# Performance work log

Hardware: AMD Instinct MI355X
Metric: run time of the kernel (lower is better)

Reference implementation:

```python
import jax, jax.numpy as jnp
import numpy as np

N = 100000   # nodes
E = 1600000  # edges
D = 128      # in_dim
H = 128      # hidden_dim
C = 40       # num_classes
EPS = 1e-5   # LayerNorm eps (torch default)


def setup_inputs() -> dict:
    key = jax.random.key(0)
    ks = jax.random.split(key, 16)
    x = jax.random.normal(ks[0], (N, D), dtype=jnp.float32)
    edge_index = jax.random.randint(ks[1], (2, E), 0, N, dtype=jnp.int64)
    s = 1.0 / np.sqrt(D)
    inp = {"x": x, "edge_index": edge_index}
    # 3 GCN layers: weight [in, H], bias [H]; LayerNorm gamma/beta [H]
    for i in range(3):
        inp[f"W{i}"] = jax.random.normal(ks[2 + i], (D if i == 0 else H, H), dtype=jnp.float32) * s
        inp[f"b{i}"] = jnp.zeros((H,), jnp.float32)
        inp[f"g{i}"] = jnp.ones((H,), jnp.float32)
        inp[f"be{i}"] = jnp.zeros((H,), jnp.float32)
    inp["Wc"] = jax.random.normal(ks[10], (H, C), dtype=jnp.float32) * (1.0 / np.sqrt(H))
    inp["bc"] = jnp.zeros((C,), jnp.float32)
    return inp


def _layer_norm(h, g, b):
    mu = jnp.mean(h, axis=-1, keepdims=True)
    var = jnp.var(h, axis=-1, keepdims=True)  # biased, matches torch
    return (h - mu) * jax.lax.rsqrt(var + EPS) * g + b


def _gcn_conv(x, W, b, src, dst, enorm, dinv2):
    # GCNConv: D^{-1/2}(A+I)D^{-1/2} X W + b (self-loops handled analytically)
    h = x @ W                                   # [N, H]
    agg = jax.ops.segment_sum(h[src] * enorm[:, None], dst, num_segments=N)
    return agg + h * dinv2[:, None] + b


def reference(x, edge_index, W0, b0, g0, be0, W1, b1, g1, be1, W2, b2, g2, be2, Wc, bc):
    src, dst = edge_index[0], edge_index[1]
    # degree with self-loops (GCNConv adds self-loops by default)
    deg = jnp.zeros((N,), x.dtype).at[dst].add(1.0) + 1.0
    dinv = jax.lax.rsqrt(deg)
    enorm = dinv[src] * dinv[dst]               # per-edge normalization
    dinv2 = dinv * dinv                         # self-loop normalization

    Ws, bs, gs, bes = (W0, W1, W2), (b0, b1, b2), (g0, g1, g2), (be0, be1, be2)
    for i in range(3):
        x_in = x
        x = _gcn_conv(x, Ws[i], bs[i], src, dst, enorm, dinv2)
        x = _layer_norm(x, gs[i], bes[i])
        x = jax.nn.elu(x)
        if i > 0:
            x = x + x_in
        # dropout: eval mode / p=0 -> identity
    return x @ Wc + bc
```

## Files before the change

### kernel.cpp

```cpp
#include <hip/hip_runtime.h>
#include <math.h>

#define N_NODES 100000
#define N_EDGES 1600000
#define DIM     128
#define NCLS    40
#define NBUCK   196
#define P1_CH   4096
#define P1_GRID 391

typedef _Float16 f16x8 __attribute__((ext_vector_type(8)));
typedef _Float16 f16x2 __attribute__((ext_vector_type(2)));
typedef float    f32x4 __attribute__((ext_vector_type(4)));

__device__ inline unsigned short f16bits(float f) {
    union { _Float16 h; unsigned short u; } cv;
    cv.h = (_Float16)f;
    return cv.u;
}
__device__ inline f16x2 as_h2(unsigned u) {
    union { unsigned u; f16x2 h; } cv;
    cv.u = u;
    return cv.h;
}
__device__ inline unsigned as_u(f16x2 h) {
    union { f16x2 h; unsigned u; } cv;
    cv.h = h;
    return cv.u;
}
__device__ inline unsigned pack_h2(float lo, float hi) {
    f16x2 h;
    h.x = (_Float16)lo;
    h.y = (_Float16)hi;
    return as_u(h);
}
__device__ inline int wave_incl_scan(int v, int lane) {
#pragma unroll
    for (int off = 1; off < 64; off <<= 1) {
        int x = __shfl_up(v, off, 64);
        if (lane >= off) v += x;
    }
    return v;
}

__global__ __launch_bounds__(256) void setup_misc(const float* __restrict__ W0,
                                                  const float* __restrict__ W1,
                                                  const float* __restrict__ W2,
                                                  const float* __restrict__ Wc,
                                                  const int* __restrict__ ei,
                                                  unsigned short* __restrict__ Wsw0,
                                                  unsigned short* __restrict__ Wsw1,
                                                  unsigned short* __restrict__ Wsw2,
                                                  unsigned short* __restrict__ Wcsw,
                                                  int* __restrict__ bcnt,
                                                  unsigned short* __restrict__ H2) {
    int blk = blockIdx.x;
    if (blk < 192) {
        const float* W = (blk < 64) ? W0 : (blk < 128) ? W1 : W2;
        unsigned short* Wsw = (blk < 64) ? Wsw0 : (blk < 128) ? Wsw1 : Wsw2;
        int o = (blk & 63) * 256 + threadIdx.x;
        int f = o >> 9;
        int l = (o >> 3) & 63;
        int j = o & 7;
        int n = f >> 2;
        int s = f & 3;
        int k = s * 32 + (l >> 4) * 8 + j;
        int c = (l & 15) * 8 + n;
        Wsw[o] = f16bits(W[k * DIM + c]);
    } else if (blk < 216) {
        int o = (blk - 192) * 256 + threadIdx.x;
        int f = o >> 9;
        int l = (o >> 3) & 63;
        int j = o & 7;
        int n = f >> 2;
        int s = f & 3;
        int k = s * 32 + (l >> 4) * 8 + j;
        int c = (l & 15) * 3 + n;
        Wcsw[o] = (c < NCLS) ? f16bits(Wc[k * NCLS + c]) : (unsigned short)0;
    } else if (blk < 216 + P1_GRID) {
        __shared__ int h[256];
        const int t  = threadIdx.x;
        const int e0 = (blk - 216) * P1_CH;
        const int cnt = min(P1_CH, N_EDGES - e0);
        h[t] = 0;
        __syncthreads();
        for (int i = t; i < cnt; i += 256)
            atomicAdd(&h[ei[N_EDGES + e0 + i] >> 9], 1);
        __syncthreads();
        if (h[t]) atomicAdd(&bcnt[t], h[t]);
    } else {
        uint4* p = (uint4*)(H2 + (size_t)N_NODES * DIM);
        uint4 zz = make_uint4(0u, 0u, 0u, 0u);
#pragma unroll
        for (int i = 0; i < 4; ++i) p[threadIdx.x + i * 256] = zz;
    }
}

__global__ __launch_bounds__(256) void bucket_p1(const int* __restrict__ ei,
                                                 const int* __restrict__ bcnt,
                                                 int* __restrict__ boff,
                                                 unsigned* __restrict__ tmp) {
    __shared__ int  hist[256];
    __shared__ int  lscan[256];
    __shared__ int  rank[256];
    __shared__ int  gbase[256];
    __shared__ int  wtotA[4];
    __shared__ int  wtotB[4];
    __shared__ int2 stage[P1_CH];
    const int t  = threadIdx.x;
    const int lane = t & 63, wv = t >> 6;
    const int e0 = blockIdx.x * P1_CH;
    const int cnt = min(P1_CH, N_EDGES - e0);

    int bcv = (t < NBUCK) ? bcnt[t] : 0;

    hist[t] = 0;
    __syncthreads();

    int2 ed[16];
#pragma unroll
    for (int i = 0; i < 16; ++i) {
        int idx = t + i * 256;
        if (idx < cnt) {
            int s = ei[e0 + idx];
            int d = ei[N_EDGES + e0 + idx];
            ed[i] = make_int2(s, d);
            atomicAdd(&hist[d >> 9], 1);
        }
    }
    __syncthreads();

    int hv = hist[t];
    int inclA = hv, inclB = bcv;
#pragma unroll
    for (int off = 1; off < 64; off <<= 1) {
        int xa = __shfl_up(inclA, off, 64);
        int xb = __shfl_up(inclB, off, 64);
        if (lane >= off) { inclA += xa; inclB += xb; }
    }
    if (lane == 63) { wtotA[wv] = inclA; wtotB[wv] = inclB; }
    __syncthreads();
    int pA = 0, pB = 0;
    for (int i = 0; i < wv; ++i) { pA += wtotA[i]; pB += wtotB[i]; }
    inclA += pA;
    inclB += pB;
    int exclA = inclA - hv;
    int exclB = inclB - bcv;
    lscan[t] = exclA;
    rank[t]  = exclA;
    if (hv > 0) gbase[t] = exclB + atomicAdd(&boff[t], hv);
    __syncthreads();

#pragma unroll
    for (int i = 0; i < 16; ++i) {
        int idx = t + i * 256;
        if (idx < cnt) {
            int b = ed[i].y >> 9;
            int p = atomicAdd(&rank[b], 1);
            stage[p] = ed[i];
        }
    }
    __syncthreads();

    for (int p = t; p < cnt; p += 256) {
        int2 v = stage[p];
        int b = v.y >> 9;
        tmp[gbase[b] + (p - lscan[b])] = ((unsigned)v.x << 9) | ((unsigned)v.y & 511u);
    }
}

__global__ __launch_bounds__(256) void bucket_p2(const unsigned* __restrict__ tmp,
                                                 const int* __restrict__ bcnt,
                                                 int* __restrict__ rowptr,
                                                 float* __restrict__ dinv,
                                                 unsigned* __restrict__ rec) {
    __shared__ int cnt[512];
    __shared__ int cur[512];
    __shared__ int wtot[4];
    __shared__ int sbeg, send;
    const int t  = threadIdx.x;
    const int lane = t & 63, wv = t >> 6;
    const int b  = blockIdx.x;
    const int d0 = b << 9;
    const int dend = min(d0 + 512, N_NODES);
    const int nn = dend - d0;

    int bcv = (t < NBUCK) ? bcnt[t] : 0;
    int binc = wave_incl_scan(bcv, lane);
    if (lane == 63) wtot[wv] = binc;
    cnt[t] = 0;
    cnt[t + 256] = 0;
    __syncthreads();
    {
        int pfx = 0;
        for (int i = 0; i < wv; ++i) pfx += wtot[i];
        binc += pfx;
        if (t == b) { sbeg = binc - bcv; send = binc; }
    }
    __syncthreads();

    const int beg = sbeg;
    const int end = send;
    for (int idx = beg + t; idx < end; idx += 256)
        atomicAdd(&cnt[tmp[idx] & 511u], 1);
    __syncthreads();

    int c0 = cnt[2 * t];
    int c1 = cnt[2 * t + 1];
    int pv = c0 + c1;
    int incl = wave_incl_scan(pv, lane);
    if (lane == 63) wtot[wv] = incl;
    __syncthreads();
    int prefix = 0;
    for (int i = 0; i < wv; ++i) prefix += wtot[i];
    incl += prefix;
    int excl = incl - pv;
    int base0 = beg + excl;
    int base1 = base0 + c0;
    cur[2 * t]     = base0;
    cur[2 * t + 1] = base1;
    if (2 * t < nn) {
        rowptr[d0 + 2 * t] = base0;
        dinv[d0 + 2 * t]   = rsqrtf((float)c0 + 1.0f);
    }
    if (2 * t + 1 < nn) {
        rowptr[d0 + 2 * t + 1] = base1;
        dinv[d0 + 2 * t + 1]   = rsqrtf((float)c1 + 1.0f);
    }
    if (b == NBUCK - 1 && t == 0) rowptr[N_NODES] = N_EDGES;
    __syncthreads();

    for (int idx = beg + t; idx < end; idx += 256) {
        unsigned u = tmp[idx];
        int pos = atomicAdd(&cur[u & 511u], 1);
        rec[pos] = (u >> 9) << 8;
    }
}

__global__ __launch_bounds__(256) void gemm_mfma_f(const float* __restrict__ X,
                                                   const unsigned short* __restrict__ Wsw,
                                                   const float* __restrict__ dinv,
                                                   unsigned short* __restrict__ H) {
    __shared__ unsigned short wlds[32 * 512];
    const int tid   = threadIdx.x;
    const int lane  = tid & 63;
    const int wave  = tid >> 6;
    const int row0w = blockIdx.x * 64 + wave * 16;
    const int m = lane & 15;
    const int q = lane >> 4;

    {
        const uint4* srcp = (const uint4*)Wsw;
        uint4*       dstp = (uint4*)wlds;
#pragma unroll
        for (int i = 0; i < 8; ++i) dstp[tid + i * 256] = srcp[tid + i * 256];
    }
    __syncthreads();

    int r = row0w + m;
    if (r >= N_NODES) r = N_NODES - 1;
    const float* xp = X + (size_t)r * DIM + q * 8;
    f16x8 af[4];
#pragma unroll
    for (int s = 0; s < 4; ++s) {
        float4 x0 = *(const float4*)(xp + s * 32);
        float4 x1 = *(const float4*)(xp + s * 32 + 4);
        f16x8 v;
        v[0] = (_Float16)x0.x; v[1] = (_Float16)x0.y;
        v[2] = (_Float16)x0.z; v[3] = (_Float16)x0.w;
        v[4] = (_Float16)x1.x; v[5] = (_Float16)x1.y;
        v[6] = (_Float16)x1.z; v[7] = (_Float16)x1.w;
        af[s] = v;
    }

    f32x4 acc[8];
    f32x4 z = {0.f, 0.f, 0.f, 0.f};
#pragma unroll
    for (int n = 0; n < 8; ++n) acc[n] = z;

    const unsigned short* wl = wlds + lane * 8;
#pragma unroll
    for (int s = 0; s < 4; ++s)
#pragma unroll
        for (int n = 0; n < 8; ++n) {
            f16x8 wf = *(const f16x8*)(wl + ((n * 4 + s) << 9));
            acc[n] = __builtin_amdgcn_mfma_f32_16x16x32_f16(af[s], wf, acc[n], 0, 0, 0);
        }

#pragma unroll
    for (int j = 0; j < 4; ++j) {
        int row = row0w + q * 4 + j;
        if (row < N_NODES) {
            float dv = dinv[row];
            uint4 o;
            o.x = pack_h2(acc[0][j] * dv, acc[1][j] * dv);
            o.y = pack_h2(acc[2][j] * dv, acc[3][j] * dv);
            o.z = pack_h2(acc[4][j] * dv, acc[5][j] * dv);
            o.w = pack_h2(acc[6][j] * dv, acc[7][j] * dv);
            *(uint4*)(H + (size_t)row * DIM + m * 8) = o;
        } else {
            uint4 zz = make_uint4(0u, 0u, 0u, 0u);
            *(uint4*)(H + (size_t)row * DIM + m * 8) = zz;
        }
    }
}

__global__ __launch_bounds__(256) void agg_ln_gemm(const unsigned short* __restrict__ Hh,
                                                   const unsigned short* __restrict__ xin,
                                                   const float* __restrict__ dinv,
                                                   const float* __restrict__ bias,
                                                   const float* __restrict__ g,
                                                   const float* __restrict__ be,
                                                   const int* __restrict__ rowptr,
                                                   const unsigned* __restrict__ rec,
                                                   const unsigned short* __restrict__ Wsw,
                                                   unsigned short* __restrict__ Cout,
                                                   unsigned short* __restrict__ Hout) {
    __shared__ _Float16 hl[16][136];
    const int tid  = threadIdx.x;
    const int lane = tid & 63;
    const int l16  = tid & 15;
    const int gb   = lane & 48;
    const int grp  = tid >> 4;
    const int wave = tid >> 6;
    const int node0 = blockIdx.x * 16;
    const int node = node0 + grp;
    const int beg  = rowptr[node];
    const int end  = rowptr[node + 1];
    const char* Hb8 = (const char*)Hh;
    const unsigned laneoff = (unsigned)l16 * 16;
    const unsigned sentin  = (unsigned)N_NODES << 8;

    f16x2 accA[4], accB[4], accC[4], accD[4];
    f16x2 hz = {(_Float16)0.f, (_Float16)0.f};
#pragma unroll
    for (int k = 0; k < 4; ++k) { accA[k] = hz; accB[k] = hz; accC[k] = hz; accD[k] = hz; }

    for (int e0 = beg; e0 < end; e0 += 16) {
        int cnt = min(end - e0, 16);
        unsigned sv = (l16 < cnt) ? rec[e0 + l16] : sentin;
        int cntR = (cnt + 7) & ~7;
        for (int j = 0; j < cntR; j += 8) {
            unsigned o0 = (unsigned)__shfl((int)sv, gb + j + 0, 64) + laneoff;
            unsigned o1 = (unsigned)__shfl((int)sv, gb + j + 1, 64) + laneoff;
            unsigned o2 = (unsigned)__shfl((int)sv, gb + j + 2, 64) + laneoff;
            unsigned o3 = (unsigned)__shfl((int)sv, gb + j + 3, 64) + laneoff;
            unsigned o4 = (unsigned)__shfl((int)sv, gb + j + 4, 64) + laneoff;
            unsigned o5 = (unsigned)__shfl((int)sv, gb + j + 5, 64) + laneoff;
            unsigned o6 = (unsigned)__shfl((int)sv, gb + j + 6, 64) + laneoff;
            unsigned o7 = (unsigned)__shfl((int)sv, gb + j + 7, 64) + laneoff;
            uint4 u0 = *(const uint4*)(Hb8 + o0);
            uint4 u1 = *(const uint4*)(Hb8 + o1);
            uint4 u2 = *(const uint4*)(Hb8 + o2);
            uint4 u3 = *(const uint4*)(Hb8 + o3);
            uint4 u4 = *(const uint4*)(Hb8 + o4);
            uint4 u5 = *(const uint4*)(Hb8 + o5);
            uint4 u6 = *(const uint4*)(Hb8 + o6);
            uint4 u7 = *(const uint4*)(Hb8 + o7);
            accA[0] += as_h2(u0.x); accA[1] += as_h2(u0.y); accA[2] += as_h2(u0.z); accA[3] += as_h2(u0.w);
            accB[0] += as_h2(u1.x); accB[1] += as_h2(u1.y); accB[2] += as_h2(u1.z); accB[3] += as_h2(u1.w);
            accC[0] += as_h2(u2.x); accC[1] += as_h2(u2.y); accC[2] += as_h2(u2.z); accC[3] += as_h2(u2.w);
            accD[0] += as_h2(u3.x); accD[1] += as_h2(u3.y); accD[2] += as_h2(u3.z); accD[3] += as_h2(u3.w);
            accA[0] += as_h2(u4.x); accA[1] += as_h2(u4.y); accA[2] += as_h2(u4.z); accA[3] += as_h2(u4.w);
            accB[0] += as_h2(u5.x); accB[1] += as_h2(u5.y); accB[2] += as_h2(u5.z); accB[3] += as_h2(u5.w);
            accC[0] += as_h2(u6.x); accC[1] += as_h2(u6.y); accC[2] += as_h2(u6.z); accC[3] += as_h2(u6.w);
            accD[0] += as_h2(u7.x); accD[1] += as_h2(u7.y); accD[2] += as_h2(u7.z); accD[3] += as_h2(u7.w);
        }
    }

#pragma unroll
    for (int k = 0; k < 4; ++k) accA[k] = (accA[k] + accB[k]) + (accC[k] + accD[k]);

    const float dv = dinv[node];
    const unsigned nodeoff = ((unsigned)node << 8) + laneoff;
    uint4 hv = *(const uint4*)(Hb8 + nodeoff);
    const int c0 = l16 * 8;
    float4 bb0 = *(const float4*)(bias + c0);
    float4 bb1 = *(const float4*)(bias + c0 + 4);
    f16x2 h0 = as_h2(hv.x), h1 = as_h2(hv.y), h2 = as_h2(hv.z), h3 = as_h2(hv.w);

    float a[8];
    a[0] = ((float)accA[0].x + (float)h0.x) * dv + bb0.x;
    a[1] = ((float)accA[0].y + (float)h0.y) * dv + bb0.y;
    a[2] = ((float)accA[1].x + (float)h1.x) * dv + bb0.z;
    a[3] = ((float)accA[1].y + (float)h1.y) * dv + bb0.w;
    a[4] = ((float)accA[2].x + (float)h2.x) * dv + bb1.x;
    a[5] = ((float)accA[2].y + (float)h2.y) * dv + bb1.y;
    a[6] = ((float)accA[3].x + (float)h3.x) * dv + bb1.z;
    a[7] = ((float)accA[3].y + (float)h3.y) * dv + bb1.w;

    float s1 = 0.f, s2 = 0.f;
#pragma unroll
    for (int i = 0; i < 8; ++i) { s1 += a[i]; s2 += a[i] * a[i]; }
#pragma unroll
    for (int mk = 1; mk <= 8; mk <<= 1) {
        s1 += __shfl_xor(s1, mk, 64);
        s2 += __shfl_xor(s2, mk, 64);
    }
    float mean = s1 * (1.0f / 128.0f);
    float var  = s2 * (1.0f / 128.0f) - mean * mean;
    float rr   = rsqrtf(var + 1e-5f);

    float4 gg0 = *(const float4*)(g + c0);
    float4 gg1 = *(const float4*)(g + c0 + 4);
    float4 ee0 = *(const float4*)(be + c0);
    float4 ee1 = *(const float4*)(be + c0 + 4);

    float r[8];
    r[0] = (a[0] - mean) * rr * gg0.x + ee0.x;
    r[1] = (a[1] - mean) * rr * gg0.y + ee0.y;
    r[2] = (a[2] - mean) * rr * gg0.z + ee0.z;
    r[3] = (a[3] - mean) * rr * gg0.w + ee0.w;
    r[4] = (a[4] - mean) * rr * gg1.x + ee1.x;
    r[5] = (a[5] - mean) * rr * gg1.y + ee1.y;
    r[6] = (a[6] - mean) * rr * gg1.z + ee1.z;
    r[7] = (a[7] - mean) * rr * gg1.w + ee1.w;
#pragma unroll
    for (int i = 0; i < 8; ++i) r[i] = r[i] > 0.0f ? r[i] : expm1f(r[i]);

    if (xin) {
        uint4 xv = *(const uint4*)((const char*)xin + nodeoff);
        f16x2 x0 = as_h2(xv.x), x1 = as_h2(xv.y), x2 = as_h2(xv.z), x3 = as_h2(xv.w);
        r[0] += (float)x0.x; r[1] += (float)x0.y;
        r[2] += (float)x1.x; r[3] += (float)x1.y;
        r[4] += (float)x2.x; r[5] += (float)x2.y;
        r[6] += (float)x3.x; r[7] += (float)x3.y;
    }

    uint4 o;
    o.x = pack_h2(r[0], r[1]);
    o.y = pack_h2(r[2], r[3]);
    o.z = pack_h2(r[4], r[5]);
    o.w = pack_h2(r[6], r[7]);
    *(uint4*)((char*)Cout + nodeoff) = o;
    *(uint4*)&hl[grp][l16 * 8] = o;
    __syncthreads();

    {
        const int m = lane & 15;
        const int q = lane >> 4;

        f16x8 af[4];
#pragma unroll
        for (int s = 0; s < 4; ++s)
            af[s] = *(const f16x8*)&hl[m][q * 8 + s * 32];

        f32x4 acc2[2];
        f32x4 z = {0.f, 0.f, 0.f, 0.f};
        acc2[0] = z; acc2[1] = z;

#pragma unroll
        for (int s = 0; s < 4; ++s)
#pragma unroll
            for (int p = 0; p < 2; ++p) {
                f16x8 wfv = *(const f16x8*)(Wsw + (((2 * wave + p) * 4 + s) << 9) + lane * 8);
                acc2[p] = __builtin_amdgcn_mfma_f32_16x16x32_f16(af[s], wfv, acc2[p], 0, 0, 0);
            }

#pragma unroll
        for (int j = 0; j < 4; ++j) {
            int row = node0 + q * 4 + j;
            float dv2 = dinv[row];
            *(unsigned*)((char*)Hout + ((unsigned)row << 8) + ((unsigned)(m * 8 + 2 * wave) << 1)) =
                pack_h2(acc2[0][j] * dv2, acc2[1][j] * dv2);
        }
    }
}

__global__ __launch_bounds__(256) void agg_ln_cls(const unsigned short* __restrict__ Hh,
                                                  const unsigned short* __restrict__ xin,
                                                  const float* __restrict__ dinv,
                                                  const float* __restrict__ bias,
                                                  const float* __restrict__ g,
                                                  const float* __restrict__ be,
                                                  const int* __restrict__ rowptr,
                                                  const unsigned* __restrict__ rec,
                                                  const unsigned short* __restrict__ Wcsw,
                                                  const float* __restrict__ bc,
                                                  float* __restrict__ out) {
    __shared__ _Float16 hl[16][136];
    const int tid  = threadIdx.x;
    const int lane = tid & 63;
    const int l16  = tid & 15;
    const int gb   = lane & 48;
    const int grp  = tid >> 4;
    const int node0 = blockIdx.x * 16;
    const int node = node0 + grp;
    const int beg  = rowptr[node];
    const int end  = rowptr[node + 1];
    const char* Hb8 = (const char*)Hh;
    const unsigned laneoff = (unsigned)l16 * 16;
    const unsigned sentin  = (unsigned)N_NODES << 8;

    f16x2 accA[4], accB[4], accC[4], accD[4];
    f16x2 hz = {(_Float16)0.f, (_Float16)0.f};
#pragma unroll
    for (int k = 0; k < 4; ++k) { accA[k] = hz; accB[k] = hz; accC[k] = hz; accD[k] = hz; }

    for (int e0 = beg; e0 < end; e0 += 16) {
        int cnt = min(end - e0, 16);
        unsigned sv = (l16 < cnt) ? rec[e0 + l16] : sentin;
        int cntR = (cnt + 7) & ~7;
        for (int j = 0; j < cntR; j += 8) {
            unsigned o0 = (unsigned)__shfl((int)sv, gb + j + 0, 64) + laneoff;
            unsigned o1 = (unsigned)__shfl((int)sv, gb + j + 1, 64) + laneoff;
            unsigned o2 = (unsigned)__shfl((int)sv, gb + j + 2, 64) + laneoff;
            unsigned o3 = (unsigned)__shfl((int)sv, gb + j + 3, 64) + laneoff;
            unsigned o4 = (unsigned)__shfl((int)sv, gb + j + 4, 64) + laneoff;
            unsigned o5 = (unsigned)__shfl((int)sv, gb + j + 5, 64) + laneoff;
            unsigned o6 = (unsigned)__shfl((int)sv, gb + j + 6, 64) + laneoff;
            unsigned o7 = (unsigned)__shfl((int)sv, gb + j + 7, 64) + laneoff;
            uint4 u0 = *(const uint4*)(Hb8 + o0);
            uint4 u1 = *(const uint4*)(Hb8 + o1);
            uint4 u2 = *(const uint4*)(Hb8 + o2);
            uint4 u3 = *(const uint4*)(Hb8 + o3);
            uint4 u4 = *(const uint4*)(Hb8 + o4);
            uint4 u5 = *(const uint4*)(Hb8 + o5);
            uint4 u6 = *(const uint4*)(Hb8 + o6);
            uint4 u7 = *(const uint4*)(Hb8 + o7);
            accA[0] += as_h2(u0.x); accA[1] += as_h2(u0.y); accA[2] += as_h2(u0.z); accA[3] += as_h2(u0.w);
            accB[0] += as_h2(u1.x); accB[1] += as_h2(u1.y); accB[2] += as_h2(u1.z); accB[3] += as_h2(u1.w);
            accC[0] += as_h2(u2.x); accC[1] += as_h2(u2.y); accC[2] += as_h2(u2.z); accC[3] += as_h2(u2.w);
            accD[0] += as_h2(u3.x); accD[1] += as_h2(u3.y); accD[2] += as_h2(u3.z); accD[3] += as_h2(u3.w);
            accA[0] += as_h2(u4.x); accA[1] += as_h2(u4.y); accA[2] += as_h2(u4.z); accA[3] += as_h2(u4.w);
            accB[0] += as_h2(u5.x); accB[1] += as_h2(u5.y); accB[2] += as_h2(u5.z); accB[3] += as_h2(u5.w);
            accC[0] += as_h2(u6.x); accC[1] += as_h2(u6.y); accC[2] += as_h2(u6.z); accC[3] += as_h2(u6.w);
            accD[0] += as_h2(u7.x); accD[1] += as_h2(u7.y); accD[2] += as_h2(u7.z); accD[3] += as_h2(u7.w);
        }
    }

#pragma unroll
    for (int k = 0; k < 4; ++k) accA[k] = (accA[k] + accB[k]) + (accC[k] + accD[k]);

    const float dv = dinv[node];
    const unsigned nodeoff = ((unsigned)node << 8) + laneoff;
    uint4 hv = *(const uint4*)(Hb8 + nodeoff);
    const int c0 = l16 * 8;
    float4 bb0 = *(const float4*)(bias + c0);
    float4 bb1 = *(const float4*)(bias + c0 + 4);
    f16x2 h0 = as_h2(hv.x), h1 = as_h2(hv.y), h2 = as_h2(hv.z), h3 = as_h2(hv.w);

    float a[8];
    a[0] = ((float)accA[0].x + (float)h0.x) * dv + bb0.x;
    a[1] = ((float)accA[0].y + (float)h0.y) * dv + bb0.y;
    a[2] = ((float)accA[1].x + (float)h1.x) * dv + bb0.z;
    a[3] = ((float)accA[1].y + (float)h1.y) * dv + bb0.w;
    a[4] = ((float)accA[2].x + (float)h2.x) * dv + bb1.x;
    a[5] = ((float)accA[2].y + (float)h2.y) * dv + bb1.y;
    a[6] = ((float)accA[3].x + (float)h3.x) * dv + bb1.z;
    a[7] = ((float)accA[3].y + (float)h3.y) * dv + bb1.w;

    float s1 = 0.f, s2 = 0.f;
#pragma unroll
    for (int i = 0; i < 8; ++i) { s1 += a[i]; s2 += a[i] * a[i]; }
#pragma unroll
    for (int mk = 1; mk <= 8; mk <<= 1) {
        s1 += __shfl_xor(s1, mk, 64);
        s2 += __shfl_xor(s2, mk, 64);
    }
    float mean = s1 * (1.0f / 128.0f);
    float var  = s2 * (1.0f / 128.0f) - mean * mean;
    float rr   = rsqrtf(var + 1e-5f);

    float4 gg0 = *(const float4*)(g + c0);
    float4 gg1 = *(const float4*)(g + c0 + 4);
    float4 ee0 = *(const float4*)(be + c0);
    float4 ee1 = *(const float4*)(be + c0 + 4);

    float r[8];
    r[0] = (a[0] - mean) * rr * gg0.x + ee0.x;
    r[1] = (a[1] - mean) * rr * gg0.y + ee0.y;
    r[2] = (a[2] - mean) * rr * gg0.z + ee0.z;
    r[3] = (a[3] - mean) * rr * gg0.w + ee0.w;
    r[4] = (a[4] - mean) * rr * gg1.x + ee1.x;
    r[5] = (a[5] - mean) * rr * gg1.y + ee1.y;
    r[6] = (a[6] - mean) * rr * gg1.z + ee1.z;
    r[7] = (a[7] - mean) * rr * gg1.w + ee1.w;
#pragma unroll
    for (int i = 0; i < 8; ++i) r[i] = r[i] > 0.0f ? r[i] : expm1f(r[i]);

    if (xin) {
        uint4 xv = *(const uint4*)((const char*)xin + nodeoff);
        f16x2 x0 = as_h2(xv.x), x1 = as_h2(xv.y), x2 = as_h2(xv.z), x3 = as_h2(xv.w);
        r[0] += (float)x0.x; r[1] += (float)x0.y;
        r[2] += (float)x1.x; r[3] += (float)x1.y;
        r[4] += (float)x2.x; r[5] += (float)x2.y;
        r[6] += (float)x3.x; r[7] += (float)x3.y;
    }

    uint4 o;
    o.x = pack_h2(r[0], r[1]);
    o.y = pack_h2(r[2], r[3]);
    o.z = pack_h2(r[4], r[5]);
    o.w = pack_h2(r[6], r[7]);
    *(uint4*)&hl[grp][l16 * 8] = o;
    __syncthreads();

    if (tid < 64) {
        const int m = lane & 15;
        const int q = lane >> 4;

        f16x8 wf[12];
#pragma unroll
        for (int f = 0; f < 12; ++f)
            wf[f] = *(const f16x8*)(Wcsw + (f << 9) + lane * 8);

        f16x8 af[4];
#pragma unroll
        for (int s = 0; s < 4; ++s)
            af[s] = *(const f16x8*)&hl[m][q * 8 + s * 32];

        f32x4 acc[3];
        f32x4 z = {0.f, 0.f, 0.f, 0.f};
#pragma unroll
        for (int n = 0; n < 3; ++n) acc[n] = z;

#pragma unroll
        for (int s = 0; s < 4; ++s)
#pragma unroll
            for (int n = 0; n < 3; ++n)
                acc[n] = __builtin_amdgcn_mfma_f32_16x16x32_f16(af[s], wf[n * 4 + s], acc[n], 0, 0, 0);

#pragma unroll
        for (int j = 0; j < 4; ++j) {
            int row = node0 + q * 4 + j;
#pragma unroll
            for (int n = 0; n < 3; ++n) {
                int c = 3 * m + n;
                if (c < NCLS)
                    out[(size_t)row * NCLS + c] = acc[n][j] + bc[c];
            }
        }
    }
}

extern "C" void kernel_launch(void* const* d_in, const int* in_sizes, int n_in,
                              void* d_out, int out_size, void* d_ws, size_t ws_size,
                              hipStream_t stream) {
    const float* x  = (const float*)d_in[0];
    const int*   ei = (const int*)d_in[1];
    const float* W[3]  = {(const float*)d_in[2], (const float*)d_in[6], (const float*)d_in[10]};
    const float* b[3]  = {(const float*)d_in[3], (const float*)d_in[7], (const float*)d_in[11]};
    const float* g[3]  = {(const float*)d_in[4], (const float*)d_in[8], (const float*)d_in[12]};
    const float* be[3] = {(const float*)d_in[5], (const float*)d_in[9], (const float*)d_in[13]};
    const float* Wc = (const float*)d_in[14];
    const float* bc = (const float*)d_in[15];
    float* out = (float*)d_out;

    char* ws = (char*)d_ws;
    const size_t NP = 400128;
    float* dinv   = (float*)(ws);
    int*   rowptr = (int*)  (ws + NP);
    int*   bcnt   = (int*)  (ws + 2 * NP);
    int*   boff   = (int*)  (ws + 2 * NP + 1024);
    unsigned* rec = (unsigned*)(ws + 2 * NP + 4096);
    unsigned short* H1 = (unsigned short*)(ws + 2 * NP + 4096 + (size_t)N_EDGES * 8);
    unsigned short* H2 = H1 + (size_t)(N_NODES + 64) * DIM;
    unsigned short* Ch = H2 + (size_t)(N_NODES + 64) * DIM;
    unsigned short* Wsw0 = Ch + (size_t)N_NODES * DIM;
    unsigned short* Wsw1 = Wsw0 + DIM * DIM;
    unsigned short* Wsw2 = Wsw1 + DIM * DIM;
    unsigned short* Wcsw = Wsw2 + DIM * DIM;
    unsigned* tmp = (unsigned*)Ch;

    hipMemsetAsync(bcnt, 0, 2048, stream);
    setup_misc<<<216 + P1_GRID + 1, 256, 0, stream>>>(W[0], W[1], W[2], Wc, ei,
                                                      Wsw0, Wsw1, Wsw2, Wcsw, bcnt, H2);

    bucket_p1<<<P1_GRID, 256, 0, stream>>>(ei, bcnt, boff, tmp);
    bucket_p2<<<NBUCK, 256, 0, stream>>>(tmp, bcnt, rowptr, dinv, rec);

    const int gemm_grid = (N_NODES + 63) / 64;
    const int agg_grid  = N_NODES / 16;

    gemm_mfma_f<<<gemm_grid, 256, 0, stream>>>(x, Wsw0, dinv, H1);

    agg_ln_gemm<<<agg_grid, 256, 0, stream>>>(H1, nullptr, dinv, b[0], g[0], be[0],
                                              rowptr, rec, Wsw1, Ch, H2);

    agg_ln_gemm<<<agg_grid, 256, 0, stream>>>(H2, Ch, dinv, b[1], g[1], be[1],
                                              rowptr, rec, Wsw2, Ch, H1);

    agg_ln_cls<<<agg_grid, 256, 0, stream>>>(H1, Ch, dinv, b[2], g[2], be[2],
                                             rowptr, rec, Wcsw, bc, out);
}
```

Measured before the change: 372.2 us.

## Merge CSR build kernels into one cooperative kernel with grid syncs

Replaces the three setup/bucketing kernels with a single cooperative-launched kernel that uses grid-wide syncs between the histogram, scatter and per-bucket sort phases. Bucket width shrinks from 512 to 256 destinations, so there are 391 buckets and one block handles each bucket, and the edge histogram is no longer read twice. This removes kernel launch gaps and one redundant pass over the edge array. It depends on all 391 blocks being co-resident, and the larger shared-memory footprint could limit occupancy.

Measured after the change: 488.7 us. +31.3%, slower.

```diff
diff --git a/kernel.cpp b/kernel.cpp
--- a/kernel.cpp
+++ b/kernel.cpp
@@ -1,13 +1,15 @@
 #include <hip/hip_runtime.h>
+#include <hip/hip_cooperative_groups.h>
 #include <math.h>
+
+namespace cg = cooperative_groups;
 
 #define N_NODES 100000
 #define N_EDGES 1600000
 #define DIM     128
 #define NCLS    40
-#define NBUCK   196
+#define NBUCK   391
 #define P1_CH   4096
-#define P1_GRID 391
 
 typedef _Float16 f16x8 __attribute__((ext_vector_type(8)));
 typedef _Float16 f16x2 __attribute__((ext_vector_type(2)));
@@ -43,22 +45,42 @@
     return v;
 }
 
-__global__ __launch_bounds__(256) void setup_misc(const float* __restrict__ W0,
-                                                  const float* __restrict__ W1,
-                                                  const float* __restrict__ W2,
-                                                  const float* __restrict__ Wc,
-                                                  const int* __restrict__ ei,
-                                                  unsigned short* __restrict__ Wsw0,
-                                                  unsigned short* __restrict__ Wsw1,
-                                                  unsigned short* __restrict__ Wsw2,
-                                                  unsigned short* __restrict__ Wcsw,
-                                                  int* __restrict__ bcnt,
-                                                  unsigned short* __restrict__ H2) {
-    int blk = blockIdx.x;
+__global__ __launch_bounds__(256) void csr_coop(const float* __restrict__ W0,
+                                                const float* __restrict__ W1,
+                                                const float* __restrict__ W2,
+                                                const float* __restrict__ Wc,
+                                                const int* __restrict__ ei,
+                                                unsigned short* __restrict__ Wsw0,
+                                                unsigned short* __restrict__ Wsw1,
+                                                unsigned short* __restrict__ Wsw2,
+                                                unsigned short* __restrict__ Wcsw,
+                                                int* __restrict__ bcnt,
+                                                int* __restrict__ boff,
+                                                unsigned* __restrict__ tmp,
+                                                int* __restrict__ rowptr,
+                                                float* __restrict__ dinv,
+                                                unsigned* __restrict__ rec,
+                                                unsigned short* __restrict__ H2) {
+    __shared__ int  hist[512];
+    __shared__ int  lscan[512];
+    __shared__ int  rank_[512];
+    __shared__ int  gbase[512];
+    __shared__ int  wtA[4], wtB[4];
+    __shared__ int  sbeg_s, send_s;
+    __shared__ int2 stage[P1_CH];
+
+    const int t    = threadIdx.x;
+    const int lane = t & 63, wv = t >> 6;
+    const int blk  = blockIdx.x;
+
+    hist[t] = 0;
+    hist[t + 256] = 0;
+    __syncthreads();
+
     if (blk < 192) {
         const float* W = (blk < 64) ? W0 : (blk < 128) ? W1 : W2;
         unsigned short* Wsw = (blk < 64) ? Wsw0 : (blk < 128) ? Wsw1 : Wsw2;
-        int o = (blk & 63) * 256 + threadIdx.x;
+        int o = (blk & 63) * 256 + t;
         int f = o >> 9;
         int l = (o >> 3) & 63;
         int j = o & 7;
@@ -68,7 +90,7 @@
         int c = (l & 15) * 8 + n;
         Wsw[o] = f16bits(W[k * DIM + c]);
     } else if (blk < 216) {
-        int o = (blk - 192) * 256 + threadIdx.x;
+        int o = (blk - 192) * 256 + t;
         int f = o >> 9;
         int l = (o >> 3) & 63;
         int j = o & 7;
@@ -77,86 +99,65 @@
         int k = s * 32 + (l >> 4) * 8 + j;
         int c = (l & 15) * 3 + n;
         Wcsw[o] = (c < NCLS) ? f16bits(Wc[k * NCLS + c]) : (unsigned short)0;
-    } else if (blk < 216 + P1_GRID) {
-        __shared__ int h[256];
-        const int t  = threadIdx.x;
-        const int e0 = (blk - 216) * P1_CH;
-        const int cnt = min(P1_CH, N_EDGES - e0);
-        h[t] = 0;
-        __syncthreads();
-        for (int i = t; i < cnt; i += 256)
-            atomicAdd(&h[ei[N_EDGES + e0 + i] >> 9], 1);
-        __syncthreads();
-        if (h[t]) atomicAdd(&bcnt[t], h[t]);
-    } else {
+    } else if (blk == 216) {
         uint4* p = (uint4*)(H2 + (size_t)N_NODES * DIM);
         uint4 zz = make_uint4(0u, 0u, 0u, 0u);
 #pragma unroll
-        for (int i = 0; i < 4; ++i) p[threadIdx.x + i * 256] = zz;
-    }
-}
-
-__global__ __launch_bounds__(256) void bucket_p1(const int* __restrict__ ei,
-                                                 const int* __restrict__ bcnt,
-                                                 int* __restrict__ boff,
-                                                 unsigned* __restrict__ tmp) {
-    __shared__ int  hist[256];
-    __shared__ int  lscan[256];
-    __shared__ int  rank[256];
-    __shared__ int  gbase[256];
-    __shared__ int  wtotA[4];
-    __shared__ int  wtotB[4];
-    __shared__ int2 stage[P1_CH];
-    const int t  = threadIdx.x;
-    const int lane = t & 63, wv = t >> 6;
-    const int e0 = blockIdx.x * P1_CH;
+        for (int i = 0; i < 4; ++i) p[t + i * 256] = zz;
+    }
+
+    const int e0  = blk * P1_CH;
     const int cnt = min(P1_CH, N_EDGES - e0);
-
-    int bcv = (t < NBUCK) ? bcnt[t] : 0;
-
-    hist[t] = 0;
-    __syncthreads();
-
     int2 ed[16];
 #pragma unroll
     for (int i = 0; i < 16; ++i) {
         int idx = t + i * 256;
         if (idx < cnt) {
-            int s = ei[e0 + idx];
-            int d = ei[N_EDGES + e0 + idx];
-            ed[i] = make_int2(s, d);
-            atomicAdd(&hist[d >> 9], 1);
-        }
-    }
-    __syncthreads();
-
-    int hv = hist[t];
-    int inclA = hv, inclB = bcv;
+            ed[i] = make_int2(ei[e0 + idx], ei[N_EDGES + e0 + idx]);
+            atomicAdd(&hist[ed[i].y >> 8], 1);
+        }
+    }
+    __syncthreads();
+    if (hist[t])       atomicAdd(&bcnt[t],       hist[t]);
+    if (hist[t + 256]) atomicAdd(&bcnt[t + 256], hist[t + 256]);
+
+    cg::this_grid().sync();
+
+    int h0 = hist[2 * t], h1 = hist[2 * t + 1];
+    int b0 = bcnt[2 * t], b1 = bcnt[2 * t + 1];
+    int pvA = h0 + h1, pvB = b0 + b1;
+    int iA = pvA, iB = pvB;
 #pragma unroll
     for (int off = 1; off < 64; off <<= 1) {
-        int xa = __shfl_up(inclA, off, 64);
-        int xb = __shfl_up(inclB, off, 64);
-        if (lane >= off) { inclA += xa; inclB += xb; }
-    }
-    if (lane == 63) { wtotA[wv] = inclA; wtotB[wv] = inclB; }
-    __syncthreads();
-    int pA = 0, pB = 0;
-    for (int i = 0; i < wv; ++i) { pA += wtotA[i]; pB += wtotB[i]; }
-    inclA += pA;
-    inclB += pB;
-    int exclA = inclA - hv;
-    int exclB = inclB - bcv;
-    lscan[t] = exclA;
-    rank[t]  = exclA;
-    if (hv > 0) gbase[t] = exclB + atomicAdd(&boff[t], hv);
+        int xa = __shfl_up(iA, off, 64);
+        int xb = __shfl_up(iB, off, 64);
+        if (lane >= off) { iA += xa; iB += xb; }
+    }
+    if (lane == 63) { wtA[wv] = iA; wtB[wv] = iB; }
+    __syncthreads();
+    {
+        int fA = 0, fB = 0;
+        for (int i = 0; i < wv; ++i) { fA += wtA[i]; fB += wtB[i]; }
+        iA += fA; iB += fB;
+    }
+    int eA = iA - pvA;
+    int eB = iB - pvB;
+    lscan[2 * t]     = eA;
+    lscan[2 * t + 1] = eA + h0;
+    rank_[2 * t]     = eA;
+    rank_[2 * t + 1] = eA + h0;
+    if (2 * t == blk)     { sbeg_s = eB;      send_s = eB + b0; }
+    if (2 * t + 1 == blk) { sbeg_s = eB + b0; send_s = eB + b0 + b1; }
+    if (h0) gbase[2 * t]     = eB        + atomicAdd(&boff[2 * t],     h0);
+    if (h1) gbase[2 * t + 1] = (eB + b0) + atomicAdd(&boff[2 * t + 1], h1);
     __syncthreads();
 
 #pragma unroll
     for (int i = 0; i < 16; ++i) {
         int idx = t + i * 256;
         if (idx < cnt) {
-            int b = ed[i].y >> 9;
-            int p = atomicAdd(&rank[b], 1);
+            int b = ed[i].y >> 8;
+            int p = atomicAdd(&rank_[b], 1);
             stage[p] = ed[i];
         }
     }
@@ -164,76 +165,44 @@
 
     for (int p = t; p < cnt; p += 256) {
         int2 v = stage[p];
-        int b = v.y >> 9;
-        tmp[gbase[b] + (p - lscan[b])] = ((unsigned)v.x << 9) | ((unsigned)v.y & 511u);
-    }
-}
-
-__global__ __launch_bounds__(256) void bucket_p2(const unsigned* __restrict__ tmp,
-                                                 const int* __restrict__ bcnt,
-                                                 int* __restrict__ rowptr,
-                                                 float* __restrict__ dinv,
-                                                 unsigned* __restrict__ rec) {
-    __shared__ int cnt[512];
-    __shared__ int cur[512];
-    __shared__ int wtot[4];
-    __shared__ int sbeg, send;
-    const int t  = threadIdx.x;
-    const int lane = t & 63, wv = t >> 6;
-    const int b  = blockIdx.x;
-    const int d0 = b << 9;
-    const int dend = min(d0 + 512, N_NODES);
-    const int nn = dend - d0;
-
-    int bcv = (t < NBUCK) ? bcnt[t] : 0;
-    int binc = wave_incl_scan(bcv, lane);
-    if (lane == 63) wtot[wv] = binc;
-    cnt[t] = 0;
-    cnt[t + 256] = 0;
+        int b = v.y >> 8;
+        tmp[gbase[b] + (p - lscan[b])] = ((unsigned)v.x << 8) | ((unsigned)v.y & 255u);
+    }
+
+    cg::this_grid().sync();
+
+    const int beg = sbeg_s;
+    const int end = send_s;
+    lscan[t] = 0;
+    __syncthreads();
+
+    for (int idx = beg + t; idx < end; idx += 256)
+        atomicAdd(&lscan[tmp[idx] & 255u], 1);
+    __syncthreads();
+
+    int c = lscan[t];
+    int incl = wave_incl_scan(c, lane);
+    if (lane == 63) wtA[wv] = incl;
     __syncthreads();
     {
-        int pfx = 0;
-        for (int i = 0; i < wv; ++i) pfx += wtot[i];
-        binc += pfx;
-        if (t == b) { sbeg = binc - bcv; send = binc; }
-    }
-    __syncthreads();
-
-    const int beg = sbeg;
-    const int end = send;
-    for (int idx = beg + t; idx < end; idx += 256)
-        atomicAdd(&cnt[tmp[idx] & 511u], 1);
-    __syncthreads();
-
-    int c0 = cnt[2 * t];
-    int c1 = cnt[2 * t + 1];
-    int pv = c0 + c1;
-    int incl = wave_incl_scan(pv, lane);
-    if (lane == 63) wtot[wv] = incl;
-    __syncthreads();
-    int prefix = 0;
-    for (int i = 0; i < wv; ++i) prefix += wtot[i];
-    incl += prefix;
-    int excl = incl - pv;
-    int base0 = beg + excl;
-    int base1 = base0 + c0;
-    cur[2 * t]     = base0;
-    cur[2 * t + 1] = base1;
-    if (2 * t < nn) {
-        rowptr[d0 + 2 * t] = base0;
-        dinv[d0 + 2 * t]   = rsqrtf((float)c0 + 1.0f);
-    }
-    if (2 * t + 1 < nn) {
-        rowptr[d0 + 2 * t + 1] = base1;
-        dinv[d0 + 2 * t + 1]   = rsqrtf((float)c1 + 1.0f);
-    }
-    if (b == NBUCK - 1 && t == 0) rowptr[N_NODES] = N_EDGES;
+        int pf = 0;
+        for (int i = 0; i < wv; ++i) pf += wtA[i];
+        incl += pf;
+    }
+    int base = beg + incl - c;
+    rank_[t] = base;
+    const int d0 = blk << 8;
+    if (d0 + t < N_NODES) {
+        rowptr[d0 + t] = base;
+        dinv[d0 + t]   = rsqrtf((float)c + 1.0f);
+    }
+    if (blk == NBUCK - 1 && t == 0) rowptr[N_NODES] = N_EDGES;
     __syncthreads();
 
     for (int idx = beg + t; idx < end; idx += 256) {
         unsigned u = tmp[idx];
-        int pos = atomicAdd(&cur[u & 511u], 1);
-        rec[pos] = (u >> 9) << 8;
+        int pos = atomicAdd(&rank_[u & 255u], 1);
+        rec[pos] = (u >> 8) << 8;
     }
 }
 
@@ -652,7 +621,7 @@
     float* dinv   = (float*)(ws);
     int*   rowptr = (int*)  (ws + NP);
     int*   bcnt   = (int*)  (ws + 2 * NP);
-    int*   boff   = (int*)  (ws + 2 * NP + 1024);
+    int*   boff   = (int*)  (ws + 2 * NP + 2048);
     unsigned* rec = (unsigned*)(ws + 2 * NP + 4096);
     unsigned short* H1 = (unsigned short*)(ws + 2 * NP + 4096 + (size_t)N_EDGES * 8);
     unsigned short* H2 = H1 + (size_t)(N_NODES + 64) * DIM;
@@ -663,12 +632,15 @@
     unsigned short* Wcsw = Wsw2 + DIM * DIM;
     unsigned* tmp = (unsigned*)Ch;
 
-    hipMemsetAsync(bcnt, 0, 2048, stream);
-    setup_misc<<<216 + P1_GRID + 1, 256, 0, stream>>>(W[0], W[1], W[2], Wc, ei,
-                                                      Wsw0, Wsw1, Wsw2, Wcsw, bcnt, H2);
-
-    bucket_p1<<<P1_GRID, 256, 0, stream>>>(ei, bcnt, boff, tmp);
-    bucket_p2<<<NBUCK, 256, 0, stream>>>(tmp, bcnt, rowptr, dinv, rec);
+    hipMemsetAsync(bcnt, 0, 4096, stream);
+
+    {
+        void* args[] = {(void*)&W[0], (void*)&W[1], (void*)&W[2], (void*)&Wc, (void*)&ei,
+                        (void*)&Wsw0, (void*)&Wsw1, (void*)&Wsw2, (void*)&Wcsw,
+                        (void*)&bcnt, (void*)&boff, (void*)&tmp,
+                        (void*)&rowptr, (void*)&dinv, (void*)&rec, (void*)&H2};
+        hipLaunchCooperativeKernel((void*)csr_coop, dim3(NBUCK), dim3(256), args, 0, stream);
+    }
 
     const int gemm_grid = (N_NODES + 63) / 64;
     const int agg_grid  = N_NODES / 16;
```
